# Kernel tuning notes

Hardware: AMD Instinct MI355X
Metric: run time of the kernel (lower is better)

Reference implementation:

```python
import jax, jax.numpy as jnp
import numpy as np

B, S, D, H = 2, 2048, 1024, 16
HD = D // H


def setup_inputs() -> dict:
    key = jax.random.key(0)
    ks = jax.random.split(key, 6)
    scale = D ** -0.5
    return {
        "x": jax.random.normal(ks[0], (B, S, D), dtype=jnp.float32),
        "attn_mask": jnp.ones((B, S), dtype=bool),
        "wq": jax.random.normal(ks[1], (D, D), dtype=jnp.float32) * scale,
        "wk": jax.random.normal(ks[2], (D, D), dtype=jnp.float32) * scale,
        "wv": jax.random.normal(ks[3], (D, D), dtype=jnp.float32) * scale,
        "wo": jax.random.normal(ks[4], (D, D), dtype=jnp.float32) * scale,
        "bo": jax.random.normal(ks[5], (D,), dtype=jnp.float32) * 0.01,
    }


def reference(x, attn_mask, wq, wk, wv, wo, bo):
    b, s, d = x.shape
    # torch Linear: y = x @ W.T
    q = (x @ wq.T).reshape(b, s, H, HD).transpose(0, 2, 1, 3)  # (b,h,s,hd)
    k = (x @ wk.T).reshape(b, s, H, HD).transpose(0, 2, 1, 3)
    v = (x @ wv.T).reshape(b, s, H, HD).transpose(0, 2, 1, 3)
    scores = jnp.einsum("bhqd,bhkd->bhqk", q, k) * (HD ** -0.5)
    causal = jnp.triu(jnp.ones((s, s), dtype=bool), k=1)  # True above diagonal
    mask = causal[None, None, :, :] | (~attn_mask)[:, None, None, :]
    mask_value = jnp.finfo(scores.dtype).min / 2
    scores = jnp.where(mask, mask_value, scores)
    att = jax.nn.softmax(scores, axis=-1)
    ctx = jnp.einsum("bhqk,bhkd->bhqd", att, v)
    ctx = ctx.transpose(0, 2, 1, 3).reshape(b, s, d)
    return ctx @ wo.T + bo
```

## Files before the change

### kernel.cpp

```cpp
#include <hip/hip_runtime.h>
#include <stdint.h>

#define SEQ   2048
#define DMODEL 1024
#define NHEAD 16
#define HDIM  64
#define MTOT  4096

typedef short s16x8 __attribute__((ext_vector_type(8)));
typedef float f32x4 __attribute__((ext_vector_type(4)));
typedef float f32x16 __attribute__((ext_vector_type(16)));
typedef unsigned u32x4 __attribute__((ext_vector_type(4)));

#define LOG2E 1.44269504088896340736f

#if __has_builtin(__builtin_amdgcn_exp2f)
#define EXP2(x) __builtin_amdgcn_exp2f(x)
#else
#define EXP2(x) exp2f(x)
#endif

#define WAITV0 asm volatile("s_waitcnt vmcnt(0)" ::: "memory")
#define WAITV3 asm volatile("s_waitcnt vmcnt(3)" ::: "memory")
#define WAITV4 asm volatile("s_waitcnt vmcnt(4)" ::: "memory")

__device__ __forceinline__ short f2bf(float f) {
  union { float f; unsigned u; } v; v.f = f;
  unsigned u = v.u + 0x7fff + ((v.u >> 16) & 1);
  return (short)(u >> 16);
}

__device__ __forceinline__ void async_cp16(const void* g, void* l) {
  __builtin_amdgcn_global_load_lds(
      (const __attribute__((address_space(1))) void*)g,
      (__attribute__((address_space(3))) void*)l, 16, 0, 0);
}

__device__ __forceinline__ f32x4 mfma16(s16x8 a, s16x8 b, f32x4 c) {
  return __builtin_amdgcn_mfma_f32_16x16x32_bf16(a, b, c, 0, 0, 0);
}
__device__ __forceinline__ f32x16 mfma32(s16x8 a, s16x8 b, f32x16 c) {
  return __builtin_amdgcn_mfma_f32_32x32x16_bf16(a, b, c, 0, 0, 0);
}

__device__ __forceinline__ void plane32swap(unsigned& a, unsigned& b) {
#if __has_builtin(__builtin_amdgcn_permlane32_swap)
  auto r = __builtin_amdgcn_permlane32_swap(a, b, false, false);
  a = r[0]; b = r[1];
#else
  asm("v_permlane32_swap_b32 %0, %1" : "+v"(a), "+v"(b));
#endif
}

__global__ __launch_bounds__(256) void cast_kernel(
    const float* __restrict__ x,  const float* __restrict__ wq,
    const float* __restrict__ wk, const float* __restrict__ wv,
    const float* __restrict__ wo,
    short* __restrict__ xb,  short* __restrict__ wqb,
    short* __restrict__ wkb, short* __restrict__ wvb, short* __restrict__ wob) {
  int i = blockIdx.x * 256 + threadIdx.x;
  const float4* src; short* dst; int off;
  const int XN = 1 << 19, WN = 1 << 17;
  if (i < XN)            { src = (const float4*)x;  dst = xb;  off = i; }
  else if (i < XN + WN)  { src = (const float4*)wq; dst = wqb; off = i - XN; }
  else if (i < XN + 2*WN){ src = (const float4*)wk; dst = wkb; off = i - XN - WN; }
  else if (i < XN + 3*WN){ src = (const float4*)wv; dst = wvb; off = i - XN - 2*WN; }
  else                   { src = (const float4*)wo; dst = wob; off = i - XN - 3*WN; }
  float4 a = src[off * 2], b = src[off * 2 + 1];
  s16x8 o;
  o[0] = f2bf(a.x); o[1] = f2bf(a.y); o[2] = f2bf(a.z); o[3] = f2bf(a.w);
  o[4] = f2bf(b.x); o[5] = f2bf(b.y); o[6] = f2bf(b.z); o[7] = f2bf(b.w);
  *(s16x8*)(dst + off * 8) = o;
}

__global__ __launch_bounds__(512, 2) void qkv_gemm(
    const short* __restrict__ xb,  const short* __restrict__ wqb,
    const short* __restrict__ wkb, const short* __restrict__ wvb,
    short* __restrict__ Q, short* __restrict__ K, short* __restrict__ Vt) {
  __shared__ short SMEM[49152];
  short (*Abuf)[4096] = reinterpret_cast<short (*)[4096]>(SMEM);
  short (*Bbuf)[3][4096] = reinterpret_cast<short (*)[3][4096]>(SMEM + 3 * 4096);
  const int tid = threadIdx.x;
  const int w = tid >> 6, lane = tid & 63;
  const int c = lane & 15, g = lane >> 4;
  const int wm = w >> 2, wn = w & 3;
  const int n0 = blockIdx.x * 128, m0 = blockIdx.y * 128;
  const int srow = lane >> 2, schunk = lane & 3;

  f32x4 acc[3][4][2] = {};

#define QKV_STAGE(KT, BS)                                                      \
  {                                                                            \
    async_cp16(xb + (m0 + w * 16 + srow) * 1024 + (KT) * 32 + schunk * 8,      \
               &Abuf[BS][w * 512]);                                            \
    async_cp16(wqb + (n0 + w * 16 + srow) * 1024 + (KT) * 32 + schunk * 8,     \
               &Bbuf[BS][0][w * 512]);                                         \
    async_cp16(wkb + (n0 + w * 16 + srow) * 1024 + (KT) * 32 + schunk * 8,     \
               &Bbuf[BS][1][w * 512]);                                         \
    async_cp16(wvb + (n0 + w * 16 + srow) * 1024 + (KT) * 32 + schunk * 8,     \
               &Bbuf[BS][2][w * 512]);                                         \
  }

  QKV_STAGE(0, 0)
  QKV_STAGE(1, 1)
  for (int kt = 0; kt < 32; ++kt) {
    if (kt < 31) { WAITV4; } else { WAITV0; }
    __builtin_amdgcn_s_barrier();
    if (kt + 2 < 32) { QKV_STAGE(kt + 2, (kt + 2) % 3) }
    const int cur = kt % 3;
    s16x8 a[4];
#pragma unroll
    for (int t = 0; t < 4; ++t)
      a[t] = *(const s16x8*)&Abuf[cur][(wm * 64 + t * 16 + c) * 32 + g * 8];
#pragma unroll
    for (int z = 0; z < 3; ++z) {
      s16x8 b[2];
#pragma unroll
      for (int u = 0; u < 2; ++u)
        b[u] = *(const s16x8*)&Bbuf[cur][z][(wn * 32 + u * 16 + c) * 32 + g * 8];
      __builtin_amdgcn_s_setprio(1);
#pragma unroll
      for (int t = 0; t < 4; ++t)
#pragma unroll
        for (int u = 0; u < 2; ++u)
          acc[z][t][u] = mfma16(a[t], b[u], acc[z][t][u]);
      __builtin_amdgcn_s_setprio(0);
    }
  }

  short* E = SMEM;
  const int b0 = m0 >> 11, sbase = m0 & 2047, hgb = n0 >> 6;

#pragma unroll
  for (int z = 0; z < 3; ++z) {
    __syncthreads();
    if (z == 2) {
#pragma unroll
      for (int t = 0; t < 4; ++t)
#pragma unroll
        for (int u = 0; u < 2; ++u) {
          int col = wn * 32 + u * 16 + c;
          int m = wm * 64 + t * 16 + g * 4;
          int phys = (m >> 3) ^ (col & 15);
          short4 o;
          o.x = f2bf(acc[z][t][u][0]); o.y = f2bf(acc[z][t][u][1]);
          o.z = f2bf(acc[z][t][u][2]); o.w = f2bf(acc[z][t][u][3]);
          *(short4*)&E[col * 128 + phys * 8 + (m & 7)] = o;
        }
      __syncthreads();
#pragma unroll
      for (int p = 0; p < 4; ++p) {
        int R = p * 32 + (tid >> 4);
        int j = tid & 15;
        int phys = j ^ (R & 15);
        s16x8 v = *(const s16x8*)&E[R * 128 + phys * 8];
        int hloc = R >> 6, hd = R & 63;
        *(s16x8*)&Vt[(((b0 * 16 + hgb + hloc) * 64 + hd) * 2048) + sbase + j * 8] = v;
      }
    } else {
      const float scale = (z == 0) ? 0.125f * LOG2E : 1.0f;
#pragma unroll
      for (int t = 0; t < 4; ++t)
#pragma unroll
        for (int u = 0; u < 2; ++u)
#pragma unroll
          for (int r = 0; r < 4; ++r) {
            int m = wm * 64 + t * 16 + g * 4 + r;
            int col = wn * 32 + u * 16 + c;
            int phys = (col >> 3) ^ ((m >> 2) & 15);
            E[m * 128 + phys * 8 + (col & 7)] = f2bf(acc[z][t][u][r] * scale);
          }
      __syncthreads();
      short* __restrict__ dst = (z == 0) ? Q : K;
#pragma unroll
      for (int p = 0; p < 4; ++p) {
        int R = p * 64 + (tid >> 3);
        int j = tid & 7;
        int m = R >> 1, hloc = R & 1;
        int phys = (hloc * 8 + j) ^ ((m >> 2) & 15);
        s16x8 v = *(const s16x8*)&E[m * 128 + phys * 8];
        *(s16x8*)&dst[(((b0 * 16 + hgb + hloc) * 2048) + sbase + m) * 64 + j * 8] = v;
      }
    }
  }
}

#define STAGE_KV(T, BS)                                                        \
  _Pragma("unroll") for (int jj = 0; jj < 2; ++jj) {                           \
    int seg = qs * 2 + jj, sub = seg >> 2, pp = seg & 3;                       \
    async_cp16(Kg + ((T) * 64 + pp * 16 + srow) * 64 + sub * 32 + sw8,         \
               &Kbuf[p][BS][sub][pp * 512]);                                   \
    async_cp16(Vg + (pp * 16 + srow) * 2048 + (T) * 64 + sub * 32 + sw8,       \
               &Vlds[p][BS][sub][pp * 512]);                                   \
  }

__global__ __launch_bounds__(512, 4) void attn_kernel(
    const short* __restrict__ Q, const short* __restrict__ K,
    const short* __restrict__ Vt, short* __restrict__ ctx) {
  __shared__ __align__(16) short Kbuf[2][2][2][64 * 32];
  __shared__ __align__(16) short Vlds[2][2][2][64 * 32];
  __shared__ float Llds[2][4][32];

  const int tid = threadIdx.x;
  const int w = tid >> 6, lane = tid & 63;
  const int n31 = lane & 31, h = lane >> 5;
  const int p = w >> 2, qs = w & 3;
  const int bh = blockIdx.x;
  int bx = blockIdx.y;
  if (bx >= 8) bx = 23 - bx;
  const int qbase = bx * 128 + qs * 32;
  const short* __restrict__ Qg = Q + bh * (SEQ * HDIM);
  const short* __restrict__ Kg = K + bh * (SEQ * HDIM);
  const short* __restrict__ Vg = Vt + bh * (SEQ * HDIM);
  const int srow = lane >> 2, schunk = lane & 3;
  const int sw8 = (schunk ^ ((srow >> 1) & 3)) * 8;
  const int rsw = (n31 >> 1) & 3;

  s16x8 qf[4];
#pragma unroll
  for (int ch = 0; ch < 4; ++ch)
    qf[ch] = *(const s16x8*)&Qg[(qbase + n31) * 64 + ch * 16 + h * 8];

  float l_run = 0.f;
  f32x16 oacc[2] = {};

  const int qlo = qbase;
  STAGE_KV(p, 0)
  for (int j = 0; j <= bx; ++j) {
    __syncthreads();
    if (j < bx) { STAGE_KV(2 * (j + 1) + p, (j + 1) & 1) }

    const short (*Kc)[64 * 32] = Kbuf[p][j & 1];
    const short (*Vc)[64 * 32] = Vlds[p][j & 1];
    const int kbase = (2 * j + p) * 64;

    unsigned pk[2][8];
#pragma unroll
    for (int mt = 0; mt < 2; ++mt) {
      const int dk = qlo - (kbase + mt * 32);
      if (dk < 0) continue;
      f32x16 st = {};
      __builtin_amdgcn_s_setprio(1);
#pragma unroll
      for (int ch = 0; ch < 4; ++ch) {
        s16x8 ka = *(const s16x8*)
            &Kc[ch >> 1][(mt * 32 + n31) * 32 + ((((ch & 1) * 2 + h) ^ rsw) * 8)];
        st = mfma32(ka, qf[ch], st);
      }
      __builtin_amdgcn_s_setprio(0);
      if (dk == 0) {
#pragma unroll
        for (int reg = 0; reg < 16; ++reg) {
          int krow = (reg & 3) + 8 * (reg >> 2) + 4 * h;
          if (krow > n31) st[reg] = -1e30f;
        }
      }
#pragma unroll
      for (int i = 0; i < 8; ++i) {
        float p0 = EXP2(st[2 * i]);
        float p1 = EXP2(st[2 * i + 1]);
        unsigned u0 = __float_as_uint(p0);
        unsigned u1 = __float_as_uint(p1);
        l_run += __uint_as_float(u0 & 0xffff0000u);
        l_run += __uint_as_float(u1 & 0xffff0000u);
        pk[mt][i] = __builtin_amdgcn_perm(u1, u0, 0x07060302u);
      }
    }

#pragma unroll
    for (int mt = 0; mt < 2; ++mt) {
      if (qlo - (kbase + mt * 32) < 0) continue;
#pragma unroll
      for (int kb2 = 0; kb2 < 2; ++kb2) {
        const int kb = mt * 2 + kb2;
        unsigned q0 = pk[mt][kb2 * 4 + 0], q1 = pk[mt][kb2 * 4 + 1];
        unsigned q2 = pk[mt][kb2 * 4 + 2], q3 = pk[mt][kb2 * 4 + 3];
        plane32swap(q0, q2);
        plane32swap(q1, q3);
        u32x4 av; av.x = q0; av.y = q1; av.z = q2; av.w = q3;
        s16x8 pa = __builtin_bit_cast(s16x8, av);
        __builtin_amdgcn_s_setprio(1);
#pragma unroll
        for (int u = 0; u < 2; ++u) {
          s16x8 vf = *(const s16x8*)
              &Vc[kb >> 1][(u * 32 + n31) * 32 + ((((kb & 1) * 2 + h) ^ rsw) * 8)];
          oacc[u] = mfma32(pa, vf, oacc[u]);
        }
        __builtin_amdgcn_s_setprio(0);
      }
    }
  }

  __syncthreads();
  float lf = l_run + __shfl_xor(l_run, 32);
  float* Ocmb = reinterpret_cast<float*>(&Kbuf[0][0][0][0]);
  if (p == 1) {
#pragma unroll
    for (int rc = 0; rc < 8; ++rc) {
      f32x4 o4;
      o4[0] = oacc[rc >> 2][(rc & 3) * 4 + 0];
      o4[1] = oacc[rc >> 2][(rc & 3) * 4 + 1];
      o4[2] = oacc[rc >> 2][(rc & 3) * 4 + 2];
      o4[3] = oacc[rc >> 2][(rc & 3) * 4 + 3];
      *(f32x4*)&Ocmb[qs * 2048 + lane * 32 + ((rc ^ (lane & 7)) << 2)] = o4;
    }
    if (h == 0) Llds[1][qs][n31] = lf;
  }
  __syncthreads();
  if (p == 0) {
#pragma unroll
    for (int rc = 0; rc < 8; ++rc) {
      f32x4 o4 = *(const f32x4*)
          &Ocmb[qs * 2048 + lane * 32 + ((rc ^ (lane & 7)) << 2)];
      oacc[rc >> 2][(rc & 3) * 4 + 0] += o4[0];
      oacc[rc >> 2][(rc & 3) * 4 + 1] += o4[1];
      oacc[rc >> 2][(rc & 3) * 4 + 2] += o4[2];
      oacc[rc >> 2][(rc & 3) * 4 + 3] += o4[3];
    }
    float lt = lf + Llds[1][qs][n31];
    if (h == 0) Llds[0][qs][n31] = lt;
    float inv[4][4];
#pragma unroll
    for (int gi = 0; gi < 4; ++gi) {
      float4 lv = *(const float4*)&Llds[0][qs][gi * 8 + 4 * h];
      inv[gi][0] = 1.0f / lv.x; inv[gi][1] = 1.0f / lv.y;
      inv[gi][2] = 1.0f / lv.z; inv[gi][3] = 1.0f / lv.w;
    }
    const int b = bh >> 4, hh = bh & 15;
#pragma unroll
    for (int u = 0; u < 2; ++u)
#pragma unroll
      for (int gi = 0; gi < 4; ++gi)
#pragma unroll
        for (int ri = 0; ri < 4; ++ri) {
          int q = qbase + 8 * gi + 4 * h + ri;
          int hd = u * 32 + n31;
          ctx[(b * 2048 + q) * 1024 + hh * 64 + hd] =
              f2bf(oacc[u][gi * 4 + ri] * inv[gi][ri]);
        }
  }
}

__global__ __launch_bounds__(256) void out_gemm(
    const short* __restrict__ ctx, const short* __restrict__ wob,
    const float* __restrict__ bo, float* __restrict__ out) {
  __shared__ short Abuf[3][128 * 32];
  __shared__ short Bbuf[3][64 * 32];
  const int tid = threadIdx.x;
  const int w = tid >> 6, lane = tid & 63;
  const int c = lane & 15, g = lane >> 4;
  const int wm = w >> 1, wn = w & 1;
  const int n0 = blockIdx.y * 64, m0 = blockIdx.x * 128;
  const int srow = lane >> 2, schunk = lane & 3;

  f32x4 acc[4][2] = {};

#define OUT_STAGE(KT, BS)                                                      \
  {                                                                            \
    _Pragma("unroll") for (int j = 0; j < 2; ++j) {                            \
      int p = w * 2 + j;                                                       \
      async_cp16(ctx + (m0 + p * 16 + srow) * 1024 + (KT) * 32 + schunk * 8,   \
                 &Abuf[BS][p * 512]);                                          \
    }                                                                          \
    async_cp16(wob + (n0 + w * 16 + srow) * 1024 + (KT) * 32 + schunk * 8,     \
               &Bbuf[BS][w * 512]);                                            \
  }

  OUT_STAGE(0, 0)
  OUT_STAGE(1, 1)
  for (int kt = 0; kt < 32; ++kt) {
    if (kt < 31) { WAITV3; } else { WAITV0; }
    __builtin_amdgcn_s_barrier();
    if (kt + 2 < 32) { OUT_STAGE(kt + 2, (kt + 2) % 3) }
    const int cur = kt % 3;
    s16x8 a[4], b[2];
#pragma unroll
    for (int t = 0; t < 4; ++t)
      a[t] = *(const s16x8*)&Abuf[cur][(wm * 64 + t * 16 + c) * 32 + g * 8];
#pragma unroll
    for (int u = 0; u < 2; ++u)
      b[u] = *(const s16x8*)&Bbuf[cur][(wn * 32 + u * 16 + c) * 32 + g * 8];
    __builtin_amdgcn_s_setprio(1);
#pragma unroll
    for (int t = 0; t < 4; ++t)
#pragma unroll
      for (int u = 0; u < 2; ++u)
        acc[t][u] = mfma16(a[t], b[u], acc[t][u]);
    __builtin_amdgcn_s_setprio(0);
  }

#pragma unroll
  for (int t = 0; t < 4; ++t)
#pragma unroll
    for (int u = 0; u < 2; ++u) {
      int col = n0 + wn * 32 + u * 16 + c;
      float bias = bo[col];
#pragma unroll
      for (int r = 0; r < 4; ++r) {
        int m = m0 + wm * 64 + t * 16 + g * 4 + r;
        out[m * 1024 + col] = acc[t][u][r] + bias;
      }
    }
}

extern "C" void kernel_launch(void* const* d_in, const int* in_sizes, int n_in,
                              void* d_out, int out_size, void* d_ws, size_t ws_size,
                              hipStream_t stream) {
  const float* x  = (const float*)d_in[0];
  const float* wq = (const float*)d_in[2];
  const float* wk = (const float*)d_in[3];
  const float* wv = (const float*)d_in[4];
  const float* wo = (const float*)d_in[5];
  const float* bo = (const float*)d_in[6];

  char* ws = (char*)d_ws;
  short* xb  = (short*)(ws);
  short* wqb = (short*)(ws + (size_t)( 8 << 20));
  short* wkb = (short*)(ws + (size_t)(10 << 20));
  short* wvb = (short*)(ws + (size_t)(12 << 20));
  short* wob = (short*)(ws + (size_t)(14 << 20));
  short* Qb  = (short*)(ws + (size_t)(16 << 20));
  short* Kb  = (short*)(ws + (size_t)(24 << 20));
  short* Vtb = (short*)(ws + (size_t)(32 << 20));
  short* ctx = (short*)(ws + (size_t)(40 << 20));
  float* out = (float*)d_out;

  cast_kernel<<<dim3(4096), dim3(256), 0, stream>>>(x, wq, wk, wv, wo,
                                                    xb, wqb, wkb, wvb, wob);
  qkv_gemm<<<dim3(8, 32), dim3(512), 0, stream>>>(xb, wqb, wkb, wvb,
                                                  Qb, Kb, Vtb);
  attn_kernel<<<dim3(32, 16), dim3(512), 0, stream>>>(Qb, Kb, Vtb, ctx);
  out_gemm<<<dim3(32, 16), dim3(256), 0, stream>>>(ctx, wob, bo, out);
}
```

Measured before the change: 168.8 us.

## Fuse fp32-to-bf16 casts of x and wo into GEMM operand loads

```diff
diff --git a/kernel.cpp b/kernel.cpp
--- a/kernel.cpp
+++ b/kernel.cpp
@@ -21,8 +21,8 @@
 #endif
 
 #define WAITV0 asm volatile("s_waitcnt vmcnt(0)" ::: "memory")
-#define WAITV3 asm volatile("s_waitcnt vmcnt(3)" ::: "memory")
 #define WAITV4 asm volatile("s_waitcnt vmcnt(4)" ::: "memory")
+#define WAITV5 asm volatile("s_waitcnt vmcnt(5)" ::: "memory")
 
 __device__ __forceinline__ short f2bf(float f) {
   union { float f; unsigned u; } v; v.f = f;
@@ -41,6 +41,16 @@
 }
 __device__ __forceinline__ f32x16 mfma32(s16x8 a, s16x8 b, f32x16 c) {
   return __builtin_amdgcn_mfma_f32_32x32x16_bf16(a, b, c, 0, 0, 0);
+}
+
+__device__ __forceinline__ s16x8 cvt8(f32x4 lo, f32x4 hi) {
+  unsigned w0, w1, w2, w3;
+  asm("v_cvt_pk_bf16_f32 %0, %1, %2" : "=v"(w0) : "v"(lo[0]), "v"(lo[1]));
+  asm("v_cvt_pk_bf16_f32 %0, %1, %2" : "=v"(w1) : "v"(lo[2]), "v"(lo[3]));
+  asm("v_cvt_pk_bf16_f32 %0, %1, %2" : "=v"(w2) : "v"(hi[0]), "v"(hi[1]));
+  asm("v_cvt_pk_bf16_f32 %0, %1, %2" : "=v"(w3) : "v"(hi[2]), "v"(hi[3]));
+  u32x4 av; av.x = w0; av.y = w1; av.z = w2; av.w = w3;
+  return __builtin_bit_cast(s16x8, av);
 }
 
 __device__ __forceinline__ void plane32swap(unsigned& a, unsigned& b) {
@@ -52,20 +62,16 @@
 #endif
 }
 
-__global__ __launch_bounds__(256) void cast_kernel(
-    const float* __restrict__ x,  const float* __restrict__ wq,
-    const float* __restrict__ wk, const float* __restrict__ wv,
-    const float* __restrict__ wo,
-    short* __restrict__ xb,  short* __restrict__ wqb,
-    short* __restrict__ wkb, short* __restrict__ wvb, short* __restrict__ wob) {
+__global__ __launch_bounds__(256) void cast_w(
+    const float* __restrict__ wq, const float* __restrict__ wk,
+    const float* __restrict__ wv,
+    short* __restrict__ wqb, short* __restrict__ wkb, short* __restrict__ wvb) {
   int i = blockIdx.x * 256 + threadIdx.x;
+  const int WN = 1 << 17;
   const float4* src; short* dst; int off;
-  const int XN = 1 << 19, WN = 1 << 17;
-  if (i < XN)            { src = (const float4*)x;  dst = xb;  off = i; }
-  else if (i < XN + WN)  { src = (const float4*)wq; dst = wqb; off = i - XN; }
-  else if (i < XN + 2*WN){ src = (const float4*)wk; dst = wkb; off = i - XN - WN; }
-  else if (i < XN + 3*WN){ src = (const float4*)wv; dst = wvb; off = i - XN - 2*WN; }
-  else                   { src = (const float4*)wo; dst = wob; off = i - XN - 3*WN; }
+  if (i < WN)            { src = (const float4*)wq; dst = wqb; off = i; }
+  else if (i < 2 * WN)   { src = (const float4*)wk; dst = wkb; off = i - WN; }
+  else                   { src = (const float4*)wv; dst = wvb; off = i - 2 * WN; }
   float4 a = src[off * 2], b = src[off * 2 + 1];
   s16x8 o;
   o[0] = f2bf(a.x); o[1] = f2bf(a.y); o[2] = f2bf(a.z); o[3] = f2bf(a.w);
@@ -74,25 +80,29 @@
 }
 
 __global__ __launch_bounds__(512, 2) void qkv_gemm(
-    const short* __restrict__ xb,  const short* __restrict__ wqb,
+    const float* __restrict__ x,   const short* __restrict__ wqb,
     const short* __restrict__ wkb, const short* __restrict__ wvb,
     short* __restrict__ Q, short* __restrict__ K, short* __restrict__ Vt) {
-  __shared__ short SMEM[49152];
-  short (*Abuf)[4096] = reinterpret_cast<short (*)[4096]>(SMEM);
-  short (*Bbuf)[3][4096] = reinterpret_cast<short (*)[3][4096]>(SMEM + 3 * 4096);
+  __shared__ __align__(16) float Afl[3][128 * 32];
+  __shared__ __align__(16) short Bbuf[3][3][4096];
   const int tid = threadIdx.x;
   const int w = tid >> 6, lane = tid & 63;
   const int c = lane & 15, g = lane >> 4;
   const int wm = w >> 2, wn = w & 3;
   const int n0 = blockIdx.x * 128, m0 = blockIdx.y * 128;
   const int srow = lane >> 2, schunk = lane & 3;
+  const int arow = lane >> 3;
+  const int aswzf = ((lane & 7) ^ arow) * 4;
+  const int e0b = (((g << 1) ^ (c & 7)) * 16);
+  const int e1b = e0b ^ 16;
 
   f32x4 acc[3][4][2] = {};
 
 #define QKV_STAGE(KT, BS)                                                      \
   {                                                                            \
-    async_cp16(xb + (m0 + w * 16 + srow) * 1024 + (KT) * 32 + schunk * 8,      \
-               &Abuf[BS][w * 512]);                                            \
+    _Pragma("unroll") for (int jj = 0; jj < 2; ++jj)                           \
+      async_cp16(x + (m0 + w * 16 + jj * 8 + arow) * 1024 + (KT) * 32 + aswzf, \
+                 (char*)Afl[BS] + w * 2048 + jj * 1024);                       \
     async_cp16(wqb + (n0 + w * 16 + srow) * 1024 + (KT) * 32 + schunk * 8,     \
                &Bbuf[BS][0][w * 512]);                                         \
     async_cp16(wkb + (n0 + w * 16 + srow) * 1024 + (KT) * 32 + schunk * 8,     \
@@ -104,14 +114,18 @@
   QKV_STAGE(0, 0)
   QKV_STAGE(1, 1)
   for (int kt = 0; kt < 32; ++kt) {
-    if (kt < 31) { WAITV4; } else { WAITV0; }
+    if (kt < 31) { WAITV5; } else { WAITV0; }
     __builtin_amdgcn_s_barrier();
     if (kt + 2 < 32) { QKV_STAGE(kt + 2, (kt + 2) % 3) }
     const int cur = kt % 3;
     s16x8 a[4];
 #pragma unroll
-    for (int t = 0; t < 4; ++t)
-      a[t] = *(const s16x8*)&Abuf[cur][(wm * 64 + t * 16 + c) * 32 + g * 8];
+    for (int t = 0; t < 4; ++t) {
+      const char* rb = (const char*)Afl[cur] + (wm * 64 + t * 16 + c) * 128;
+      f32x4 lo = *(const f32x4*)(rb + e0b);
+      f32x4 hi = *(const f32x4*)(rb + e1b);
+      a[t] = cvt8(lo, hi);
+    }
 #pragma unroll
     for (int z = 0; z < 3; ++z) {
       s16x8 b[2];
@@ -128,7 +142,7 @@
     }
   }
 
-  short* E = SMEM;
+  short* E = (short*)Afl;
   const int b0 = m0 >> 11, sbase = m0 & 2047, hgb = n0 >> 6;
 
 #pragma unroll
@@ -342,34 +356,39 @@
 }
 
 __global__ __launch_bounds__(256) void out_gemm(
-    const short* __restrict__ ctx, const short* __restrict__ wob,
+    const short* __restrict__ ctx, const float* __restrict__ wo,
     const float* __restrict__ bo, float* __restrict__ out) {
   __shared__ short Abuf[3][128 * 32];
-  __shared__ short Bbuf[3][64 * 32];
+  __shared__ __align__(16) float Bfl[3][64 * 32];
   const int tid = threadIdx.x;
   const int w = tid >> 6, lane = tid & 63;
   const int c = lane & 15, g = lane >> 4;
   const int wm = w >> 1, wn = w & 1;
   const int n0 = blockIdx.y * 64, m0 = blockIdx.x * 128;
   const int srow = lane >> 2, schunk = lane & 3;
+  const int arow = lane >> 3;
+  const int aswzf = ((lane & 7) ^ arow) * 4;
+  const int e0b = (((g << 1) ^ (c & 7)) * 16);
+  const int e1b = e0b ^ 16;
 
   f32x4 acc[4][2] = {};
 
 #define OUT_STAGE(KT, BS)                                                      \
   {                                                                            \
     _Pragma("unroll") for (int j = 0; j < 2; ++j) {                            \
-      int p = w * 2 + j;                                                       \
-      async_cp16(ctx + (m0 + p * 16 + srow) * 1024 + (KT) * 32 + schunk * 8,   \
-                 &Abuf[BS][p * 512]);                                          \
+      int pp = w * 2 + j;                                                      \
+      async_cp16(ctx + (m0 + pp * 16 + srow) * 1024 + (KT) * 32 + schunk * 8,  \
+                 &Abuf[BS][pp * 512]);                                         \
     }                                                                          \
-    async_cp16(wob + (n0 + w * 16 + srow) * 1024 + (KT) * 32 + schunk * 8,     \
-               &Bbuf[BS][w * 512]);                                            \
+    _Pragma("unroll") for (int j = 0; j < 2; ++j)                              \
+      async_cp16(wo + (n0 + w * 16 + j * 8 + arow) * 1024 + (KT) * 32 + aswzf, \
+                 (char*)Bfl[BS] + w * 2048 + j * 1024);                        \
   }
 
   OUT_STAGE(0, 0)
   OUT_STAGE(1, 1)
   for (int kt = 0; kt < 32; ++kt) {
-    if (kt < 31) { WAITV3; } else { WAITV0; }
+    if (kt < 31) { WAITV4; } else { WAITV0; }
     __builtin_amdgcn_s_barrier();
     if (kt + 2 < 32) { OUT_STAGE(kt + 2, (kt + 2) % 3) }
     const int cur = kt % 3;
@@ -378,8 +397,12 @@
     for (int t = 0; t < 4; ++t)
       a[t] = *(const s16x8*)&Abuf[cur][(wm * 64 + t * 16 + c) * 32 + g * 8];
 #pragma unroll
-    for (int u = 0; u < 2; ++u)
-      b[u] = *(const s16x8*)&Bbuf[cur][(wn * 32 + u * 16 + c) * 32 + g * 8];
+    for (int u = 0; u < 2; ++u) {
+      const char* rb = (const char*)Bfl[cur] + (wn * 32 + u * 16 + c) * 128;
+      f32x4 lo = *(const f32x4*)(rb + e0b);
+      f32x4 hi = *(const f32x4*)(rb + e1b);
+      b[u] = cvt8(lo, hi);
+    }
     __builtin_amdgcn_s_setprio(1);
 #pragma unroll
     for (int t = 0; t < 4; ++t)
@@ -414,21 +437,18 @@
   const float* bo = (const float*)d_in[6];
 
   char* ws = (char*)d_ws;
-  short* xb  = (short*)(ws);
-  short* wqb = (short*)(ws + (size_t)( 8 << 20));
-  short* wkb = (short*)(ws + (size_t)(10 << 20));
-  short* wvb = (short*)(ws + (size_t)(12 << 20));
-  short* wob = (short*)(ws + (size_t)(14 << 20));
+  short* wqb = (short*)(ws + (size_t)(10 << 20));
+  short* wkb = (short*)(ws + (size_t)(12 << 20));
+  short* wvb = (short*)(ws + (size_t)(14 << 20));
   short* Qb  = (short*)(ws + (size_t)(16 << 20));
   short* Kb  = (short*)(ws + (size_t)(24 << 20));
   short* Vtb = (short*)(ws + (size_t)(32 << 20));
   short* ctx = (short*)(ws + (size_t)(40 << 20));
   float* out = (float*)d_out;
 
-  cast_kernel<<<dim3(4096), dim3(256), 0, stream>>>(x, wq, wk, wv, wo,
-                                                    xb, wqb, wkb, wvb, wob);
-  qkv_gemm<<<dim3(8, 32), dim3(512), 0, stream>>>(xb, wqb, wkb, wvb,
+  cast_w<<<dim3(1536), dim3(256), 0, stream>>>(wq, wk, wv, wqb, wkb, wvb);
+  qkv_gemm<<<dim3(8, 32), dim3(512), 0, stream>>>(x, wqb, wkb, wvb,
                                                   Qb, Kb, Vtb);
   attn_kernel<<<dim3(32, 16), dim3(512), 0, stream>>>(Qb, Kb, Vtb, ctx);
-  out_gemm<<<dim3(32, 16), dim3(256), 0, stream>>>(ctx, wob, bo, out);
-}
+  out_gemm<<<dim3(32, 16), dim3(256), 0, stream>>>(ctx, wo, bo, out);
+}
```

New measurement: 187.2 us. 10.9% more time.

## Double qkv_gemm block to 1024 threads, halving per-warp M tile

Applied to the files above, without the earlier changes.

```diff
diff --git a/kernel.cpp b/kernel.cpp
--- a/kernel.cpp
+++ b/kernel.cpp
@@ -21,8 +21,8 @@
 #endif
 
 #define WAITV0 asm volatile("s_waitcnt vmcnt(0)" ::: "memory")
+#define WAITV2 asm volatile("s_waitcnt vmcnt(2)" ::: "memory")
 #define WAITV3 asm volatile("s_waitcnt vmcnt(3)" ::: "memory")
-#define WAITV4 asm volatile("s_waitcnt vmcnt(4)" ::: "memory")
 
 __device__ __forceinline__ short f2bf(float f) {
   union { float f; unsigned u; } v; v.f = f;
@@ -73,7 +73,7 @@
   *(s16x8*)(dst + off * 8) = o;
 }
 
-__global__ __launch_bounds__(512, 2) void qkv_gemm(
+__global__ __launch_bounds__(1024, 4) void qkv_gemm(
     const short* __restrict__ xb,  const short* __restrict__ wqb,
     const short* __restrict__ wkb, const short* __restrict__ wvb,
     short* __restrict__ Q, short* __restrict__ K, short* __restrict__ Vt) {
@@ -86,32 +86,36 @@
   const int wm = w >> 2, wn = w & 3;
   const int n0 = blockIdx.x * 128, m0 = blockIdx.y * 128;
   const int srow = lane >> 2, schunk = lane & 3;
-
-  f32x4 acc[3][4][2] = {};
+  const int w8 = w & 7;
+
+  f32x4 acc[3][2][2] = {};
 
 #define QKV_STAGE(KT, BS)                                                      \
   {                                                                            \
-    async_cp16(xb + (m0 + w * 16 + srow) * 1024 + (KT) * 32 + schunk * 8,      \
-               &Abuf[BS][w * 512]);                                            \
-    async_cp16(wqb + (n0 + w * 16 + srow) * 1024 + (KT) * 32 + schunk * 8,     \
-               &Bbuf[BS][0][w * 512]);                                         \
-    async_cp16(wkb + (n0 + w * 16 + srow) * 1024 + (KT) * 32 + schunk * 8,     \
-               &Bbuf[BS][1][w * 512]);                                         \
-    async_cp16(wvb + (n0 + w * 16 + srow) * 1024 + (KT) * 32 + schunk * 8,     \
-               &Bbuf[BS][2][w * 512]);                                         \
+    if (w < 8) {                                                               \
+      async_cp16(xb + (m0 + w8 * 16 + srow) * 1024 + (KT) * 32 + schunk * 8,   \
+                 &Abuf[BS][w8 * 512]);                                         \
+      async_cp16(wkb + (n0 + w8 * 16 + srow) * 1024 + (KT) * 32 + schunk * 8,  \
+                 &Bbuf[BS][1][w8 * 512]);                                      \
+    } else {                                                                   \
+      async_cp16(wqb + (n0 + w8 * 16 + srow) * 1024 + (KT) * 32 + schunk * 8,  \
+                 &Bbuf[BS][0][w8 * 512]);                                      \
+      async_cp16(wvb + (n0 + w8 * 16 + srow) * 1024 + (KT) * 32 + schunk * 8,  \
+                 &Bbuf[BS][2][w8 * 512]);                                      \
+    }                                                                          \
   }
 
   QKV_STAGE(0, 0)
   QKV_STAGE(1, 1)
   for (int kt = 0; kt < 32; ++kt) {
-    if (kt < 31) { WAITV4; } else { WAITV0; }
+    if (kt < 31) { WAITV2; } else { WAITV0; }
     __builtin_amdgcn_s_barrier();
     if (kt + 2 < 32) { QKV_STAGE(kt + 2, (kt + 2) % 3) }
     const int cur = kt % 3;
-    s16x8 a[4];
-#pragma unroll
-    for (int t = 0; t < 4; ++t)
-      a[t] = *(const s16x8*)&Abuf[cur][(wm * 64 + t * 16 + c) * 32 + g * 8];
+    s16x8 a[2];
+#pragma unroll
+    for (int t = 0; t < 2; ++t)
+      a[t] = *(const s16x8*)&Abuf[cur][(wm * 32 + t * 16 + c) * 32 + g * 8];
 #pragma unroll
     for (int z = 0; z < 3; ++z) {
       s16x8 b[2];
@@ -120,7 +124,7 @@
         b[u] = *(const s16x8*)&Bbuf[cur][z][(wn * 32 + u * 16 + c) * 32 + g * 8];
       __builtin_amdgcn_s_setprio(1);
 #pragma unroll
-      for (int t = 0; t < 4; ++t)
+      for (int t = 0; t < 2; ++t)
 #pragma unroll
         for (int u = 0; u < 2; ++u)
           acc[z][t][u] = mfma16(a[t], b[u], acc[z][t][u]);
@@ -136,11 +140,11 @@
     __syncthreads();
     if (z == 2) {
 #pragma unroll
-      for (int t = 0; t < 4; ++t)
+      for (int t = 0; t < 2; ++t)
 #pragma unroll
         for (int u = 0; u < 2; ++u) {
           int col = wn * 32 + u * 16 + c;
-          int m = wm * 64 + t * 16 + g * 4;
+          int m = wm * 32 + t * 16 + g * 4;
           int phys = (m >> 3) ^ (col & 15);
           short4 o;
           o.x = f2bf(acc[z][t][u][0]); o.y = f2bf(acc[z][t][u][1]);
@@ -149,8 +153,8 @@
         }
       __syncthreads();
 #pragma unroll
-      for (int p = 0; p < 4; ++p) {
-        int R = p * 32 + (tid >> 4);
+      for (int p = 0; p < 2; ++p) {
+        int R = p * 64 + (tid >> 4);
         int j = tid & 15;
         int phys = j ^ (R & 15);
         s16x8 v = *(const s16x8*)&E[R * 128 + phys * 8];
@@ -160,12 +164,12 @@
     } else {
       const float scale = (z == 0) ? 0.125f * LOG2E : 1.0f;
 #pragma unroll
-      for (int t = 0; t < 4; ++t)
+      for (int t = 0; t < 2; ++t)
 #pragma unroll
         for (int u = 0; u < 2; ++u)
 #pragma unroll
           for (int r = 0; r < 4; ++r) {
-            int m = wm * 64 + t * 16 + g * 4 + r;
+            int m = wm * 32 + t * 16 + g * 4 + r;
             int col = wn * 32 + u * 16 + c;
             int phys = (col >> 3) ^ ((m >> 2) & 15);
             E[m * 128 + phys * 8 + (col & 7)] = f2bf(acc[z][t][u][r] * scale);
@@ -173,8 +177,8 @@
       __syncthreads();
       short* __restrict__ dst = (z == 0) ? Q : K;
 #pragma unroll
-      for (int p = 0; p < 4; ++p) {
-        int R = p * 64 + (tid >> 3);
+      for (int p = 0; p < 2; ++p) {
+        int R = p * 128 + (tid >> 3);
         int j = tid & 7;
         int m = R >> 1, hloc = R & 1;
         int phys = (hloc * 8 + j) ^ ((m >> 2) & 15);
@@ -358,9 +362,9 @@
 #define OUT_STAGE(KT, BS)                                                      \
   {                                                                            \
     _Pragma("unroll") for (int j = 0; j < 2; ++j) {                            \
-      int p = w * 2 + j;                                                       \
-      async_cp16(ctx + (m0 + p * 16 + srow) * 1024 + (KT) * 32 + schunk * 8,   \
-                 &Abuf[BS][p * 512]);                                          \
+      int pp = w * 2 + j;                                                      \
+      async_cp16(ctx + (m0 + pp * 16 + srow) * 1024 + (KT) * 32 + schunk * 8,  \
+                 &Abuf[BS][pp * 512]);                                         \
     }                                                                          \
     async_cp16(wob + (n0 + w * 16 + srow) * 1024 + (KT) * 32 + schunk * 8,     \
                &Bbuf[BS][w * 512]);                                            \
@@ -427,8 +431,8 @@
 
   cast_kernel<<<dim3(4096), dim3(256), 0, stream>>>(x, wq, wk, wv, wo,
                                                     xb, wqb, wkb, wvb, wob);
-  qkv_gemm<<<dim3(8, 32), dim3(512), 0, stream>>>(xb, wqb, wkb, wvb,
-                                                  Qb, Kb, Vtb);
+  qkv_gemm<<<dim3(8, 32), dim3(1024), 0, stream>>>(xb, wqb, wkb, wvb,
+                                                   Qb, Kb, Vtb);
   attn_kernel<<<dim3(32, 16), dim3(512), 0, stream>>>(Qb, Kb, Vtb, ctx);
   out_gemm<<<dim3(32, 16), dim3(256), 0, stream>>>(ctx, wob, bo, out);
 }
```

New measurement: 170.7 us. Within noise of the previous version (+1.1%).
